# Kernel optimization log

Measured on AMD Instinct MI355X. Metric: run time of the kernel, lower is better.

The kernel has to match this reference:

```python
import jax, jax.numpy as jnp
import numpy as np
from jax import lax

T, H = 4096, 2048          # tokens, hidden_size
E, K = 64, 8               # n_routed_experts, top_k
I = 512                    # moe_intermediate_size
IS = 512                   # shared intermediate = moe_intermediate_size * n_shared_experts
ROUTED_SCALING = 2.5


def setup_inputs() -> dict:
    key = jax.random.key(0)
    ks = jax.random.split(key, 6)
    return {
        "hidden_states": jax.random.normal(ks[0], (T, H), jnp.float32),
        "gate_w": jax.random.normal(ks[1], (H, E), jnp.float32) * 0.05,
        "w13": jax.random.normal(ks[2], (E, H, 2 * I), jnp.float32) * 0.02,
        "w2": jax.random.normal(ks[3], (E, I, H), jnp.float32) * 0.02,
        "shared_w13": jax.random.normal(ks[4], (H, 2 * IS), jnp.float32) * 0.02,
        "shared_w2": jax.random.normal(ks[5], (IS, H), jnp.float32) * 0.02,
    }


def reference(hidden_states, gate_w, w13, w2, shared_w13, shared_w2):
    # --- router: sigmoid scoring, grouped top-k with 1 group == plain top-k ---
    logits = hidden_states @ gate_w                        # [T, E]
    scores = jax.nn.sigmoid(logits.astype(jnp.float32))
    topk_w, topk_ids = lax.top_k(scores, K)                # [T, K]
    topk_w = topk_w / jnp.sum(topk_w, axis=-1, keepdims=True)  # renormalize

    # --- dispatch: sort token-expert pairs by expert id, grouped GEMM ---
    flat_ids = topk_ids.reshape(-1)                        # [T*K]
    order = jnp.argsort(flat_ids)                          # pairs grouped by expert
    token_idx = order // K                                 # source token of each sorted pair
    x_sorted = hidden_states[token_idx]                    # [T*K, H]
    group_sizes = jnp.bincount(flat_ids, length=E).astype(jnp.int32)

    gu = lax.ragged_dot(x_sorted, w13, group_sizes)        # [T*K, 2I]
    h = jax.nn.silu(gu[:, :I]) * gu[:, I:]                 # SiluAndMul
    out_sorted = lax.ragged_dot(h, w2, group_sizes)        # [T*K, H]

    # --- combine: unsort, weight, sum over top-k ---
    inv = jnp.argsort(order)
    out_pairs = out_sorted[inv].reshape(T, K, H)
    routed = jnp.sum(out_pairs * topk_w[..., None].astype(out_pairs.dtype), axis=1)

    # --- shared expert MLP ---
    sg = hidden_states @ shared_w13                        # [T, 2*IS]
    shared = (jax.nn.silu(sg[:, :IS]) * sg[:, IS:]) @ shared_w2

    return routed * ROUTED_SCALING + shared
```

## Files before the change

### kernel.cpp

```cpp
#include <hip/hip_runtime.h>
#include <hip/hip_bf16.h>

#define T_TOK 4096
#define HD    2048
#define NE    64
#define TOPK  8
#define IMID  512
#define N13   1024
#define NPAIR (T_TOK*TOPK)
#define NROWS (NPAIR + T_TOK)
#define MAXT2 208
#define RSCALE 2.5f

typedef __attribute__((ext_vector_type(8))) __bf16 bf16x8;
typedef __attribute__((ext_vector_type(4))) float  f32x4;

__global__ __launch_bounds__(256) void init_kernel(float4* __restrict__ out4,
                                                   int* __restrict__ counts,
                                                   int* __restrict__ curs) {
  int gid = blockIdx.x * 256 + threadIdx.x;
  float4 z; z.x = z.y = z.z = z.w = 0.f;
  out4[gid] = z;
  if (gid < NE + 1) { counts[gid] = 0; curs[gid] = 0; }
}

__global__ __launch_bounds__(256) void cvt_kernel(const float4* __restrict__ hs4,
                                                  bf16x8* __restrict__ hb8) {
  int gid = blockIdx.x * 256 + threadIdx.x;
  float4 a = hs4[2 * gid], b = hs4[2 * gid + 1];
  bf16x8 v = { (__bf16)a.x, (__bf16)a.y, (__bf16)a.z, (__bf16)a.w,
               (__bf16)b.x, (__bf16)b.y, (__bf16)b.z, (__bf16)b.w };
  hb8[gid] = v;
}

__global__ __launch_bounds__(256) void logits_kernel(const float* __restrict__ hs,
                                                     const float* __restrict__ gw,
                                                     float* __restrict__ logits) {
  __shared__ float hsm[64][16];
  __shared__ float gwm[64][64];
  int tid = threadIdx.x;
  int tb = blockIdx.x * 16;
  int tok = tid >> 4, e4 = (tid & 15) * 4;
  float acc[4] = {0.f, 0.f, 0.f, 0.f};
  for (int c = 0; c < 32; ++c) {
    int kb = c * 64;
    {
      int t16 = tid & 15, kq = tid >> 4;
      float4 f = *(const float4*)&hs[(size_t)(tb + t16) * HD + kb + kq * 4];
      hsm[kq * 4 + 0][t16] = f.x; hsm[kq * 4 + 1][t16] = f.y;
      hsm[kq * 4 + 2][t16] = f.z; hsm[kq * 4 + 3][t16] = f.w;
#pragma unroll
      for (int it = 0; it < 4; ++it) {
        int q = tid + it * 256;
        int gr = q >> 4, gc = (q & 15) * 4;
        *(float4*)&gwm[gr][gc] = *(const float4*)&gw[(size_t)(kb + gr) * NE + gc];
      }
    }
    __syncthreads();
#pragma unroll 8
    for (int k = 0; k < 64; ++k) {
      float h = hsm[k][tok];
      float4 g = *(const float4*)&gwm[k][e4];
      acc[0] += h * g.x; acc[1] += h * g.y; acc[2] += h * g.z; acc[3] += h * g.w;
    }
    __syncthreads();
  }
#pragma unroll
  for (int j = 0; j < 4; ++j) logits[(size_t)(tb + tok) * NE + e4 + j] = acc[j];
}

__global__ __launch_bounds__(256) void top8_kernel(const float* __restrict__ logits,
                                                   int* __restrict__ topk_id,
                                                   float* __restrict__ pair_w,
                                                   int* __restrict__ counts) {
  int lane = threadIdx.x & 63;
  int t = blockIdx.x * 4 + (threadIdx.x >> 6);
  float v = logits[(size_t)t * NE + lane];
  float s = 1.f / (1.f + __expf(-v));
  float cur = s, ssum = 0.f;
  int myid = 0; float myw = 0.f;
  for (int k = 0; k < TOPK; ++k) {
    float bv = cur; int bi = lane;
#pragma unroll
    for (int off = 32; off >= 1; off >>= 1) {
      float ov = __shfl_xor(bv, off);
      int   oi = __shfl_xor(bi, off);
      if (ov > bv || (ov == bv && oi < bi)) { bv = ov; bi = oi; }
    }
    ssum += bv;
    if (lane == k) { myid = bi; myw = bv; }
    if (lane == bi) cur = -1.f;
  }
  if (lane < TOPK) {
    topk_id[(size_t)t * TOPK + lane] = myid;
    pair_w[(size_t)t * TOPK + lane] = myw / ssum * RSCALE;
    atomicAdd(&counts[myid], 1);
  }
}

__global__ void scan_kernel(const int* __restrict__ counts, int* __restrict__ offs,
                            int2* __restrict__ tiles) {
  __shared__ int cnt[65], pref[66], tp[66];
  int tid = threadIdx.x;
  if (tid < 64) cnt[tid] = counts[tid];
  if (tid == 64) cnt[64] = T_TOK;
  __syncthreads();
  if (tid == 0) {
    int o = 0, t = 0;
    for (int e = 0; e <= 64; ++e) {
      pref[e] = o; tp[e] = t;
      o += cnt[e]; t += (cnt[e] + 255) >> 8;
    }
    pref[65] = o; tp[65] = t;
  }
  __syncthreads();
  if (tid <= 64) {
    offs[tid] = pref[tid];
    int c = cnt[tid], base = pref[tid], tb = tp[tid];
    int nt = (c + 255) >> 8;
    for (int i = 0; i < nt; ++i) {
      int rr = c - i * 256; if (rr > 256) rr = 256;
      tiles[tb + i] = make_int2(base + i * 256, (tid << 16) | rr);
    }
  }
  __syncthreads();
  for (int i = tp[65] + tid; i < MAXT2; i += 128) tiles[i] = make_int2(0, 0);
}

__global__ __launch_bounds__(256) void scatter_kernel(const int* __restrict__ topk_id,
                                                      const float* __restrict__ pair_w,
                                                      const int* __restrict__ offs,
                                                      int* __restrict__ curs,
                                                      int* __restrict__ row_token,
                                                      float* __restrict__ row_w) {
  int p = blockIdx.x * 256 + threadIdx.x;
  int dst, t; float w;
  if (p < NPAIR) {
    t = p >> 3; int e = topk_id[p]; w = pair_w[p];
    dst = offs[e] + atomicAdd(&curs[e], 1);
  } else {
    t = p - NPAIR; w = 1.0f;
    dst = NPAIR + t;
  }
  row_token[dst] = t;
  row_w[dst] = w;
}

__device__ __forceinline__ int swz(int row, int kbyte) {
  return row * 128 + (kbyte ^ ((row & 7) << 4));
}
__device__ __forceinline__ void glds16(const void* g, void* l) {
  __builtin_amdgcn_global_load_lds((const __attribute__((address_space(1))) void*)g,
                                   (__attribute__((address_space(3))) void*)l, 16, 0, 0);
}
__device__ __forceinline__ void store_bx8(__bf16* Bs, int col, int kbyte, const float* p) {
  bf16x8 v = { (__bf16)p[0], (__bf16)p[1], (__bf16)p[2], (__bf16)p[3],
               (__bf16)p[4], (__bf16)p[5], (__bf16)p[6], (__bf16)p[7] };
  *(bf16x8*)&Bs[swz(col, kbyte) >> 1] = v;
}

__global__ __launch_bounds__(1024, 4) void gemm1_kernel(const __bf16* __restrict__ hidden_bf,
                                                        const float* __restrict__ w13,
                                                        const float* __restrict__ sw13,
                                                        const int* __restrict__ row_token,
                                                        const int2* __restrict__ tiles,
                                                        __bf16* __restrict__ hbuf) {
  int2 td = tiles[blockIdx.y];
  int rows = td.y & 0xFFFF;
  if (rows == 0) return;
  int e = td.y >> 16, row0 = td.x;
  const float* W = (e < NE) ? (w13 + (size_t)e * (HD * N13)) : sw13;
  int n0 = blockIdx.x * 64;

  __shared__ __bf16 As[2][256 * 64];
  __shared__ __bf16 Bgs[2][64 * 64];
  __shared__ __bf16 Bus[2][64 * 64];

  int tid = threadIdx.x;
  int lane = tid & 63, wv = tid >> 6;
  int wrow = wv >> 1, wc = wv & 1;
  int l15 = lane & 15, lq = lane >> 4;

  int kswz = (((lane & 7) ^ ((lane >> 3) & 7)) << 3);
  const __bf16* Abase[2];
#pragma unroll
  for (int i = 0; i < 2; ++i) {
    int grow = row0 + wv * 16 + i * 8 + (lane >> 3);
    if (grow >= NROWS) grow = NROWS - 1;
    Abase[i] = hidden_bf + (size_t)row_token[grow] * HD + kswz;
  }
  int bm = tid >> 9, bcol = tid & 63, bkq = (tid >> 6) & 7;
  const float* Bp0 = W + (size_t)(bkq * 8) * N13 + n0 + bm * 512 + bcol;
  __bf16* Bmy[2];
  Bmy[0] = bm ? Bus[0] : Bgs[0];
  Bmy[1] = bm ? Bus[1] : Bgs[1];

  float p[8];
#pragma unroll
  for (int r = 0; r < 8; ++r) p[r] = Bp0[(size_t)r * N13];
#pragma unroll
  for (int i = 0; i < 2; ++i) glds16(Abase[i], &As[0][wv * 1024 + i * 512]);
  store_bx8(Bmy[0], bcol, bkq * 16, p);
  asm volatile("s_waitcnt vmcnt(0) lgkmcnt(0)" ::: "memory");
  __builtin_amdgcn_s_barrier();
  __builtin_amdgcn_sched_barrier(0);

  f32x4 accg[2][2], accu[2][2];
#pragma unroll
  for (int i = 0; i < 2; ++i)
#pragma unroll
    for (int j = 0; j < 2; ++j) { accg[i][j] = (f32x4)(0.f); accu[i][j] = (f32x4)(0.f); }

  for (int s = 0; s < 32; ++s) {
    int cur = s & 1;
    if (s + 1 < 32) {
      const float* Bp2 = Bp0 + (size_t)(s + 1) * 64 * N13;
#pragma unroll
      for (int r = 0; r < 8; ++r) p[r] = Bp2[(size_t)r * N13];
    }
    __builtin_amdgcn_sched_barrier(0);
    if (s + 1 < 32) {
#pragma unroll
      for (int i = 0; i < 2; ++i)
        glds16(Abase[i] + (s + 1) * 64, &As[cur ^ 1][wv * 1024 + i * 512]);
    }
    __builtin_amdgcn_sched_barrier(0);
#pragma unroll
    for (int kk = 0; kk < 2; ++kk) {
      int koff = kk * 64 + lq * 16;
      bf16x8 a[2], bg[2], bu[2];
#pragma unroll
      for (int i = 0; i < 2; ++i)
        a[i] = *(const bf16x8*)&As[cur][swz(wrow * 32 + i * 16 + l15, koff) >> 1];
#pragma unroll
      for (int j = 0; j < 2; ++j) {
        bg[j] = *(const bf16x8*)&Bgs[cur][swz(wc * 32 + j * 16 + l15, koff) >> 1];
        bu[j] = *(const bf16x8*)&Bus[cur][swz(wc * 32 + j * 16 + l15, koff) >> 1];
      }
#pragma unroll
      for (int i = 0; i < 2; ++i)
#pragma unroll
        for (int j = 0; j < 2; ++j) {
          accg[i][j] = __builtin_amdgcn_mfma_f32_16x16x32_bf16(a[i], bg[j], accg[i][j], 0, 0, 0);
          accu[i][j] = __builtin_amdgcn_mfma_f32_16x16x32_bf16(a[i], bu[j], accu[i][j], 0, 0, 0);
        }
    }
    if (s + 1 < 32)
      store_bx8(Bmy[cur ^ 1], bcol, bkq * 16, p);
    asm volatile("s_waitcnt vmcnt(0) lgkmcnt(0)" ::: "memory");
    __builtin_amdgcn_s_barrier();
    __builtin_amdgcn_sched_barrier(0);
  }
#pragma unroll
  for (int mi = 0; mi < 2; ++mi) {
#pragma unroll
    for (int r = 0; r < 4; ++r) {
      int rl = wrow * 32 + mi * 16 + lq * 4 + r;
      if (rl < rows) {
        size_t hrow = (size_t)(row0 + rl) * IMID;
#pragma unroll
        for (int j = 0; j < 2; ++j) {
          float g = accg[mi][j][r], u = accu[mi][j][r];
          float hv = g * u / (1.f + __expf(-g));
          hbuf[hrow + n0 + wc * 32 + j * 16 + l15] = (__bf16)hv;
        }
      }
    }
  }
}

__global__ __launch_bounds__(1024, 4) void gemm2_kernel(const __bf16* __restrict__ hbuf,
                                                        const float* __restrict__ w2,
                                                        const float* __restrict__ sw2,
                                                        const int* __restrict__ row_token,
                                                        const float* __restrict__ row_w,
                                                        const int2* __restrict__ tiles,
                                                        float* __restrict__ out) {
  int2 td = tiles[blockIdx.y];
  int rows = td.y & 0xFFFF;
  if (rows == 0) return;
  int e = td.y >> 16, row0 = td.x;
  const float* W = (e < NE) ? (w2 + (size_t)e * (IMID * HD)) : sw2;
  int n0 = blockIdx.x * 128;

  __shared__ __bf16 As[2][256 * 64];
  __shared__ __bf16 Bs[2][128 * 64];

  int tid = threadIdx.x;
  int lane = tid & 63, wv = tid >> 6;
  int wr = wv >> 2, wc = wv & 3;
  int l15 = lane & 15, lq = lane >> 4;

  int kswz = (((lane & 7) ^ ((lane >> 3) & 7)) << 3);
  const __bf16* Abase[2];
#pragma unroll
  for (int i = 0; i < 2; ++i) {
    int grow = row0 + wv * 16 + i * 8 + (lane >> 3);
    if (grow >= NROWS) grow = NROWS - 1;
    Abase[i] = hbuf + (size_t)grow * IMID + kswz;
  }
  int bcol = tid & 127, bkq = tid >> 7;
  const float* Bp0 = W + (size_t)(bkq * 8) * HD + n0 + bcol;

  float p[8];
#pragma unroll
  for (int r = 0; r < 8; ++r) p[r] = Bp0[(size_t)r * HD];
#pragma unroll
  for (int i = 0; i < 2; ++i) glds16(Abase[i], &As[0][wv * 1024 + i * 512]);
  store_bx8(Bs[0], bcol, bkq * 16, p);
  asm volatile("s_waitcnt vmcnt(0) lgkmcnt(0)" ::: "memory");
  __builtin_amdgcn_s_barrier();
  __builtin_amdgcn_sched_barrier(0);

  f32x4 acc[4][2];
#pragma unroll
  for (int i = 0; i < 4; ++i)
#pragma unroll
    for (int j = 0; j < 2; ++j) acc[i][j] = (f32x4)(0.f);

  for (int s = 0; s < 8; ++s) {
    int cur = s & 1;
    if (s + 1 < 8) {
      const float* Bp2 = Bp0 + (size_t)(s + 1) * 64 * HD;
#pragma unroll
      for (int r = 0; r < 8; ++r) p[r] = Bp2[(size_t)r * HD];
    }
    __builtin_amdgcn_sched_barrier(0);
    if (s + 1 < 8) {
#pragma unroll
      for (int i = 0; i < 2; ++i)
        glds16(Abase[i] + (s + 1) * 64, &As[cur ^ 1][wv * 1024 + i * 512]);
    }
    __builtin_amdgcn_sched_barrier(0);
#pragma unroll
    for (int kk = 0; kk < 2; ++kk) {
      int koff = kk * 64 + lq * 16;
      bf16x8 a[4], b[2];
#pragma unroll
      for (int i = 0; i < 4; ++i)
        a[i] = *(const bf16x8*)&As[cur][swz(wr * 64 + i * 16 + l15, koff) >> 1];
#pragma unroll
      for (int j = 0; j < 2; ++j)
        b[j] = *(const bf16x8*)&Bs[cur][swz(wc * 32 + j * 16 + l15, koff) >> 1];
#pragma unroll
      for (int i = 0; i < 4; ++i)
#pragma unroll
        for (int j = 0; j < 2; ++j)
          acc[i][j] = __builtin_amdgcn_mfma_f32_16x16x32_bf16(a[i], b[j], acc[i][j], 0, 0, 0);
    }
    if (s + 1 < 8)
      store_bx8(Bs[cur ^ 1], bcol, bkq * 16, p);
    asm volatile("s_waitcnt vmcnt(0) lgkmcnt(0)" ::: "memory");
    __builtin_amdgcn_s_barrier();
    __builtin_amdgcn_sched_barrier(0);
  }
#pragma unroll
  for (int i = 0; i < 4; ++i) {
#pragma unroll
    for (int r = 0; r < 4; ++r) {
      int rl = wr * 64 + i * 16 + lq * 4 + r;
      if (rl < rows) {
        int gr = row0 + rl;
        int tok = row_token[gr];
        float wgt = row_w[gr];
        float* orow = out + (size_t)tok * HD + n0 + wc * 32;
#pragma unroll
        for (int j = 0; j < 2; ++j)
          atomicAdd(&orow[j * 16 + l15], acc[i][j][r] * wgt);
      }
    }
  }
}

extern "C" void kernel_launch(void* const* d_in, const int* in_sizes, int n_in,
                              void* d_out, int out_size, void* d_ws, size_t ws_size,
                              hipStream_t stream) {
  const float* hidden = (const float*)d_in[0];
  const float* gate_w = (const float*)d_in[1];
  const float* w13    = (const float*)d_in[2];
  const float* w2     = (const float*)d_in[3];
  const float* sw13   = (const float*)d_in[4];
  const float* sw2    = (const float*)d_in[5];
  float* out = (float*)d_out;

  char* ws = (char*)d_ws;
  size_t off = 0;
  __bf16* hbuf      = (__bf16*)(ws + off); off += (size_t)NROWS * IMID * 2;
  __bf16* hidden_bf = (__bf16*)(ws + off); off += (size_t)T_TOK * HD * 2;
  float* logits  = (float*)(ws + off);  off += (size_t)T_TOK * NE * 4;
  int*   topk_id = (int*)(ws + off);    off += (size_t)NPAIR * 4;
  float* pair_w  = (float*)(ws + off);  off += (size_t)NPAIR * 4;
  int*   row_tok = (int*)(ws + off);    off += (size_t)NROWS * 4;
  float* row_w   = (float*)(ws + off);  off += (size_t)NROWS * 4;
  int*   counts  = (int*)(ws + off);    off += 512;
  int*   curs    = (int*)(ws + off);    off += 512;
  int*   offs    = (int*)(ws + off);    off += 512;
  int2*  tiles   = (int2*)(ws + off);   off += MAXT2 * 8;

  init_kernel<<<T_TOK * HD / 4 / 256, 256, 0, stream>>>((float4*)out, counts, curs);
  cvt_kernel<<<T_TOK * HD / 8 / 256, 256, 0, stream>>>((const float4*)hidden, (bf16x8*)hidden_bf);
  logits_kernel<<<T_TOK / 16, 256, 0, stream>>>(hidden, gate_w, logits);
  top8_kernel<<<T_TOK / 4, 256, 0, stream>>>(logits, topk_id, pair_w, counts);
  scan_kernel<<<1, 128, 0, stream>>>(counts, offs, tiles);
  scatter_kernel<<<NROWS / 256, 256, 0, stream>>>(topk_id, pair_w, offs, curs, row_tok, row_w);
  gemm1_kernel<<<dim3(8, MAXT2), 1024, 0, stream>>>(hidden_bf, w13, sw13, row_tok, tiles, hbuf);
  gemm2_kernel<<<dim3(16, MAXT2), 1024, 0, stream>>>(hbuf, w2, sw2, row_tok, row_w, tiles, out);
}
```

Before: 848.7 us.

## Widen GEMM N-tiles, switch to 32x32x16 MFMA, and remap blocks per XCD

Both grouped GEMM kernels now use wider N tiles: 128 gate plus 128 up columns in gemm1, and 256 columns in gemm2. They switch from 16x16x32 to 32x32x16 bf16 MFMA with 16-float accumulators. Block indices are remapped so each XCD handles a fixed N slice across tiles, which should improve L2 reuse of expert weights. Wider tiles halve the grid and cut redundant A-row gathers, and setprio raises wave priority around the MFMA section. The cost is more LDS and registers per block, possibly lowering occupancy under launch_bounds(1024,4).

```diff
diff --git a/kernel.cpp b/kernel.cpp
--- a/kernel.cpp
+++ b/kernel.cpp
@@ -12,8 +12,8 @@
 #define MAXT2 208
 #define RSCALE 2.5f
 
-typedef __attribute__((ext_vector_type(8))) __bf16 bf16x8;
-typedef __attribute__((ext_vector_type(4))) float  f32x4;
+typedef __attribute__((ext_vector_type(8)))  __bf16 bf16x8;
+typedef __attribute__((ext_vector_type(16))) float  f32x16;
 
 __global__ __launch_bounds__(256) void init_kernel(float4* __restrict__ out4,
                                                    int* __restrict__ counts,
@@ -165,21 +165,25 @@
                                                         const int* __restrict__ row_token,
                                                         const int2* __restrict__ tiles,
                                                         __bf16* __restrict__ hbuf) {
-  int2 td = tiles[blockIdx.y];
+  int lin = blockIdx.x + 4 * blockIdx.y;
+  int xcd = lin & 7, local = lin >> 3;
+  int ns = xcd & 3;
+  int tix = ((xcd >> 2) * 104) + local;
+  int2 td = tiles[tix];
   int rows = td.y & 0xFFFF;
   if (rows == 0) return;
   int e = td.y >> 16, row0 = td.x;
   const float* W = (e < NE) ? (w13 + (size_t)e * (HD * N13)) : sw13;
-  int n0 = blockIdx.x * 64;
+  int n0 = ns * 128;
 
   __shared__ __bf16 As[2][256 * 64];
-  __shared__ __bf16 Bgs[2][64 * 64];
-  __shared__ __bf16 Bus[2][64 * 64];
+  __shared__ __bf16 Bgs[2][128 * 64];
+  __shared__ __bf16 Bus[2][128 * 64];
 
   int tid = threadIdx.x;
   int lane = tid & 63, wv = tid >> 6;
-  int wrow = wv >> 1, wc = wv & 1;
-  int l15 = lane & 15, lq = lane >> 4;
+  int wr = wv >> 2, wc = wv & 3;
+  int l31 = lane & 31, lh = lane >> 5;
 
   int kswz = (((lane & 7) ^ ((lane >> 3) & 7)) << 3);
   const __bf16* Abase[2];
@@ -189,34 +193,33 @@
     if (grow >= NROWS) grow = NROWS - 1;
     Abase[i] = hidden_bf + (size_t)row_token[grow] * HD + kswz;
   }
-  int bm = tid >> 9, bcol = tid & 63, bkq = (tid >> 6) & 7;
-  const float* Bp0 = W + (size_t)(bkq * 8) * N13 + n0 + bm * 512 + bcol;
-  __bf16* Bmy[2];
-  Bmy[0] = bm ? Bus[0] : Bgs[0];
-  Bmy[1] = bm ? Bus[1] : Bgs[1];
-
-  float p[8];
-#pragma unroll
-  for (int r = 0; r < 8; ++r) p[r] = Bp0[(size_t)r * N13];
+  int bm = tid >> 9, bcol = tid & 127, bkq2 = (tid >> 7) & 3;
+  const float* Bp0 = W + (size_t)(bkq2 * 16) * N13 + (bm ? 512 + n0 : n0) + bcol;
+
+  float p[16];
+#pragma unroll
+  for (int r = 0; r < 16; ++r) p[r] = Bp0[(size_t)r * N13];
 #pragma unroll
   for (int i = 0; i < 2; ++i) glds16(Abase[i], &As[0][wv * 1024 + i * 512]);
-  store_bx8(Bmy[0], bcol, bkq * 16, p);
+  {
+    __bf16* Bmy = bm ? Bus[0] : Bgs[0];
+    store_bx8(Bmy, bcol, bkq2 * 32, p);
+    store_bx8(Bmy, bcol, bkq2 * 32 + 16, p + 8);
+  }
   asm volatile("s_waitcnt vmcnt(0) lgkmcnt(0)" ::: "memory");
   __builtin_amdgcn_s_barrier();
   __builtin_amdgcn_sched_barrier(0);
 
-  f32x4 accg[2][2], accu[2][2];
-#pragma unroll
-  for (int i = 0; i < 2; ++i)
-#pragma unroll
-    for (int j = 0; j < 2; ++j) { accg[i][j] = (f32x4)(0.f); accu[i][j] = (f32x4)(0.f); }
+  f32x16 accg[2], accu[2];
+#pragma unroll
+  for (int i = 0; i < 2; ++i) { accg[i] = (f32x16)(0.f); accu[i] = (f32x16)(0.f); }
 
   for (int s = 0; s < 32; ++s) {
     int cur = s & 1;
     if (s + 1 < 32) {
       const float* Bp2 = Bp0 + (size_t)(s + 1) * 64 * N13;
 #pragma unroll
-      for (int r = 0; r < 8; ++r) p[r] = Bp2[(size_t)r * N13];
+      for (int r = 0; r < 16; ++r) p[r] = Bp2[(size_t)r * N13];
     }
     __builtin_amdgcn_sched_barrier(0);
     if (s + 1 < 32) {
@@ -225,45 +228,39 @@
         glds16(Abase[i] + (s + 1) * 64, &As[cur ^ 1][wv * 1024 + i * 512]);
     }
     __builtin_amdgcn_sched_barrier(0);
-#pragma unroll
-    for (int kk = 0; kk < 2; ++kk) {
-      int koff = kk * 64 + lq * 16;
-      bf16x8 a[2], bg[2], bu[2];
-#pragma unroll
-      for (int i = 0; i < 2; ++i)
-        a[i] = *(const bf16x8*)&As[cur][swz(wrow * 32 + i * 16 + l15, koff) >> 1];
-#pragma unroll
-      for (int j = 0; j < 2; ++j) {
-        bg[j] = *(const bf16x8*)&Bgs[cur][swz(wc * 32 + j * 16 + l15, koff) >> 1];
-        bu[j] = *(const bf16x8*)&Bus[cur][swz(wc * 32 + j * 16 + l15, koff) >> 1];
-      }
-#pragma unroll
-      for (int i = 0; i < 2; ++i)
-#pragma unroll
-        for (int j = 0; j < 2; ++j) {
-          accg[i][j] = __builtin_amdgcn_mfma_f32_16x16x32_bf16(a[i], bg[j], accg[i][j], 0, 0, 0);
-          accu[i][j] = __builtin_amdgcn_mfma_f32_16x16x32_bf16(a[i], bu[j], accu[i][j], 0, 0, 0);
-        }
-    }
-    if (s + 1 < 32)
-      store_bx8(Bmy[cur ^ 1], bcol, bkq * 16, p);
+    __builtin_amdgcn_s_setprio(1);
+#pragma unroll
+    for (int ks = 0; ks < 4; ++ks) {
+      int kbyte = ks * 32 + lh * 16;
+      bf16x8 a0 = *(const bf16x8*)&As[cur][swz(wr * 64 + l31,      kbyte) >> 1];
+      bf16x8 a1 = *(const bf16x8*)&As[cur][swz(wr * 64 + 32 + l31, kbyte) >> 1];
+      bf16x8 bg = *(const bf16x8*)&Bgs[cur][swz(wc * 32 + l31, kbyte) >> 1];
+      bf16x8 bu = *(const bf16x8*)&Bus[cur][swz(wc * 32 + l31, kbyte) >> 1];
+      accg[0] = __builtin_amdgcn_mfma_f32_32x32x16_bf16(a0, bg, accg[0], 0, 0, 0);
+      accg[1] = __builtin_amdgcn_mfma_f32_32x32x16_bf16(a1, bg, accg[1], 0, 0, 0);
+      accu[0] = __builtin_amdgcn_mfma_f32_32x32x16_bf16(a0, bu, accu[0], 0, 0, 0);
+      accu[1] = __builtin_amdgcn_mfma_f32_32x32x16_bf16(a1, bu, accu[1], 0, 0, 0);
+    }
+    __builtin_amdgcn_s_setprio(0);
+    if (s + 1 < 32) {
+      __bf16* Bmy = bm ? Bus[cur ^ 1] : Bgs[cur ^ 1];
+      store_bx8(Bmy, bcol, bkq2 * 32, p);
+      store_bx8(Bmy, bcol, bkq2 * 32 + 16, p + 8);
+    }
     asm volatile("s_waitcnt vmcnt(0) lgkmcnt(0)" ::: "memory");
     __builtin_amdgcn_s_barrier();
     __builtin_amdgcn_sched_barrier(0);
   }
 #pragma unroll
-  for (int mi = 0; mi < 2; ++mi) {
-#pragma unroll
-    for (int r = 0; r < 4; ++r) {
-      int rl = wrow * 32 + mi * 16 + lq * 4 + r;
+  for (int i = 0; i < 2; ++i) {
+#pragma unroll
+    for (int r = 0; r < 16; ++r) {
+      int rloc = (r & 3) + 8 * (r >> 2) + 4 * lh;
+      int rl = wr * 64 + i * 32 + rloc;
       if (rl < rows) {
-        size_t hrow = (size_t)(row0 + rl) * IMID;
-#pragma unroll
-        for (int j = 0; j < 2; ++j) {
-          float g = accg[mi][j][r], u = accu[mi][j][r];
-          float hv = g * u / (1.f + __expf(-g));
-          hbuf[hrow + n0 + wc * 32 + j * 16 + l15] = (__bf16)hv;
-        }
+        float g = accg[i][r], u = accu[i][r];
+        float hv = g * u / (1.f + __expf(-g));
+        hbuf[(size_t)(row0 + rl) * IMID + n0 + wc * 32 + l31] = (__bf16)hv;
       }
     }
   }
@@ -276,20 +273,23 @@
                                                         const float* __restrict__ row_w,
                                                         const int2* __restrict__ tiles,
                                                         float* __restrict__ out) {
-  int2 td = tiles[blockIdx.y];
+  int lin = blockIdx.x + 8 * blockIdx.y;
+  int xcd = lin & 7, local = lin >> 3;
+  int ns = xcd, tix = local;
+  int2 td = tiles[tix];
   int rows = td.y & 0xFFFF;
   if (rows == 0) return;
   int e = td.y >> 16, row0 = td.x;
   const float* W = (e < NE) ? (w2 + (size_t)e * (IMID * HD)) : sw2;
-  int n0 = blockIdx.x * 128;
+  int n0 = ns * 256;
 
   __shared__ __bf16 As[2][256 * 64];
-  __shared__ __bf16 Bs[2][128 * 64];
+  __shared__ __bf16 Bs[2][256 * 64];
 
   int tid = threadIdx.x;
   int lane = tid & 63, wv = tid >> 6;
   int wr = wv >> 2, wc = wv & 3;
-  int l15 = lane & 15, lq = lane >> 4;
+  int l31 = lane & 31, lh = lane >> 5;
 
   int kswz = (((lane & 7) ^ ((lane >> 3) & 7)) << 3);
   const __bf16* Abase[2];
@@ -299,31 +299,32 @@
     if (grow >= NROWS) grow = NROWS - 1;
     Abase[i] = hbuf + (size_t)grow * IMID + kswz;
   }
-  int bcol = tid & 127, bkq = tid >> 7;
-  const float* Bp0 = W + (size_t)(bkq * 8) * HD + n0 + bcol;
-
-  float p[8];
-#pragma unroll
-  for (int r = 0; r < 8; ++r) p[r] = Bp0[(size_t)r * HD];
+  int bcol = tid & 255, bkq2 = tid >> 8;
+  const float* Bp0 = W + (size_t)(bkq2 * 16) * HD + n0 + bcol;
+
+  float p[16];
+#pragma unroll
+  for (int r = 0; r < 16; ++r) p[r] = Bp0[(size_t)r * HD];
 #pragma unroll
   for (int i = 0; i < 2; ++i) glds16(Abase[i], &As[0][wv * 1024 + i * 512]);
-  store_bx8(Bs[0], bcol, bkq * 16, p);
+  store_bx8(Bs[0], bcol, bkq2 * 32, p);
+  store_bx8(Bs[0], bcol, bkq2 * 32 + 16, p + 8);
   asm volatile("s_waitcnt vmcnt(0) lgkmcnt(0)" ::: "memory");
   __builtin_amdgcn_s_barrier();
   __builtin_amdgcn_sched_barrier(0);
 
-  f32x4 acc[4][2];
-#pragma unroll
-  for (int i = 0; i < 4; ++i)
-#pragma unroll
-    for (int j = 0; j < 2; ++j) acc[i][j] = (f32x4)(0.f);
+  f32x16 acc[2][2];
+#pragma unroll
+  for (int i = 0; i < 2; ++i)
+#pragma unroll
+    for (int j = 0; j < 2; ++j) acc[i][j] = (f32x16)(0.f);
 
   for (int s = 0; s < 8; ++s) {
     int cur = s & 1;
     if (s + 1 < 8) {
       const float* Bp2 = Bp0 + (size_t)(s + 1) * 64 * HD;
 #pragma unroll
-      for (int r = 0; r < 8; ++r) p[r] = Bp2[(size_t)r * HD];
+      for (int r = 0; r < 16; ++r) p[r] = Bp2[(size_t)r * HD];
     }
     __builtin_amdgcn_sched_barrier(0);
     if (s + 1 < 8) {
@@ -332,41 +333,41 @@
         glds16(Abase[i] + (s + 1) * 64, &As[cur ^ 1][wv * 1024 + i * 512]);
     }
     __builtin_amdgcn_sched_barrier(0);
-#pragma unroll
-    for (int kk = 0; kk < 2; ++kk) {
-      int koff = kk * 64 + lq * 16;
-      bf16x8 a[4], b[2];
-#pragma unroll
-      for (int i = 0; i < 4; ++i)
-        a[i] = *(const bf16x8*)&As[cur][swz(wr * 64 + i * 16 + l15, koff) >> 1];
-#pragma unroll
-      for (int j = 0; j < 2; ++j)
-        b[j] = *(const bf16x8*)&Bs[cur][swz(wc * 32 + j * 16 + l15, koff) >> 1];
-#pragma unroll
-      for (int i = 0; i < 4; ++i)
-#pragma unroll
-        for (int j = 0; j < 2; ++j)
-          acc[i][j] = __builtin_amdgcn_mfma_f32_16x16x32_bf16(a[i], b[j], acc[i][j], 0, 0, 0);
-    }
-    if (s + 1 < 8)
-      store_bx8(Bs[cur ^ 1], bcol, bkq * 16, p);
+    __builtin_amdgcn_s_setprio(1);
+#pragma unroll
+    for (int ks = 0; ks < 4; ++ks) {
+      int kbyte = ks * 32 + lh * 16;
+      bf16x8 a0 = *(const bf16x8*)&As[cur][swz(wr * 64 + l31,      kbyte) >> 1];
+      bf16x8 a1 = *(const bf16x8*)&As[cur][swz(wr * 64 + 32 + l31, kbyte) >> 1];
+      bf16x8 b0 = *(const bf16x8*)&Bs[cur][swz(wc * 64 + l31,      kbyte) >> 1];
+      bf16x8 b1 = *(const bf16x8*)&Bs[cur][swz(wc * 64 + 32 + l31, kbyte) >> 1];
+      acc[0][0] = __builtin_amdgcn_mfma_f32_32x32x16_bf16(a0, b0, acc[0][0], 0, 0, 0);
+      acc[0][1] = __builtin_amdgcn_mfma_f32_32x32x16_bf16(a0, b1, acc[0][1], 0, 0, 0);
+      acc[1][0] = __builtin_amdgcn_mfma_f32_32x32x16_bf16(a1, b0, acc[1][0], 0, 0, 0);
+      acc[1][1] = __builtin_amdgcn_mfma_f32_32x32x16_bf16(a1, b1, acc[1][1], 0, 0, 0);
+    }
+    __builtin_amdgcn_s_setprio(0);
+    if (s + 1 < 8) {
+      store_bx8(Bs[cur ^ 1], bcol, bkq2 * 32, p);
+      store_bx8(Bs[cur ^ 1], bcol, bkq2 * 32 + 16, p + 8);
+    }
     asm volatile("s_waitcnt vmcnt(0) lgkmcnt(0)" ::: "memory");
     __builtin_amdgcn_s_barrier();
     __builtin_amdgcn_sched_barrier(0);
   }
 #pragma unroll
-  for (int i = 0; i < 4; ++i) {
-#pragma unroll
-    for (int r = 0; r < 4; ++r) {
-      int rl = wr * 64 + i * 16 + lq * 4 + r;
+  for (int i = 0; i < 2; ++i) {
+#pragma unroll
+    for (int r = 0; r < 16; ++r) {
+      int rloc = (r & 3) + 8 * (r >> 2) + 4 * lh;
+      int rl = wr * 64 + i * 32 + rloc;
       if (rl < rows) {
         int gr = row0 + rl;
         int tok = row_token[gr];
         float wgt = row_w[gr];
-        float* orow = out + (size_t)tok * HD + n0 + wc * 32;
-#pragma unroll
-        for (int j = 0; j < 2; ++j)
-          atomicAdd(&orow[j * 16 + l15], acc[i][j][r] * wgt);
+        float* orow = out + (size_t)tok * HD + n0 + wc * 64;
+        atomicAdd(&orow[l31],      acc[i][0][r] * wgt);
+        atomicAdd(&orow[32 + l31], acc[i][1][r] * wgt);
       }
     }
   }
@@ -403,6 +404,6 @@
   top8_kernel<<<T_TOK / 4, 256, 0, stream>>>(logits, topk_id, pair_w, counts);
   scan_kernel<<<1, 128, 0, stream>>>(counts, offs, tiles);
   scatter_kernel<<<NROWS / 256, 256, 0, stream>>>(topk_id, pair_w, offs, curs, row_tok, row_w);
-  gemm1_kernel<<<dim3(8, MAXT2), 1024, 0, stream>>>(hidden_bf, w13, sw13, row_tok, tiles, hbuf);
-  gemm2_kernel<<<dim3(16, MAXT2), 1024, 0, stream>>>(hbuf, w2, sw2, row_tok, row_w, tiles, out);
-}
+  gemm1_kernel<<<dim3(4, MAXT2), 1024, 0, stream>>>(hidden_bf, w13, sw13, row_tok, tiles, hbuf);
+  gemm2_kernel<<<dim3(8, MAXT2), 1024, 0, stream>>>(hbuf, w2, sw2, row_tok, row_w, tiles, out);
+}
```

Result: slower. 894.2 us (+5.4%).

## Triple-buffer A tiles in grouped GEMMs and replace atomic combine with gather kernel

Applied to the files above, without the earlier changes.

Both grouped GEMM kernels now prefetch two k-steps ahead, using three A buffers in LDS and two register sets for B. A partial vmcnt wait replaces the full drain, and MFMA sections run at raised wave priority, so memory latency overlaps compute better. When the workspace is large enough, gemm2 writes weighted per-pair rows to a buffer and a separate combine kernel sums each token's 8 pairs plus the shared row. This removes the float atomics and the output zeroing pass, at the cost of about 300 MB of extra writes and reads and more LDS per block.

```diff
diff --git a/kernel.cpp b/kernel.cpp
--- a/kernel.cpp
+++ b/kernel.cpp
@@ -12,16 +12,15 @@
 #define MAXT2 208
 #define RSCALE 2.5f
 
-typedef __attribute__((ext_vector_type(8))) __bf16 bf16x8;
-typedef __attribute__((ext_vector_type(4))) float  f32x4;
-
-__global__ __launch_bounds__(256) void init_kernel(float4* __restrict__ out4,
-                                                   int* __restrict__ counts,
-                                                   int* __restrict__ curs) {
-  int gid = blockIdx.x * 256 + threadIdx.x;
-  float4 z; z.x = z.y = z.z = z.w = 0.f;
-  out4[gid] = z;
-  if (gid < NE + 1) { counts[gid] = 0; curs[gid] = 0; }
+typedef __attribute__((ext_vector_type(8)))  __bf16 bf16x8;
+typedef __attribute__((ext_vector_type(4)))  float  f32x4;
+
+__global__ void init_small(int* __restrict__ counts, int* __restrict__ curs) {
+  int tid = threadIdx.x;
+  if (tid < NE + 1) { counts[tid] = 0; curs[tid] = 0; }
+}
+__global__ __launch_bounds__(256) void zero_out_kernel(float4* __restrict__ out4) {
+  out4[blockIdx.x * 256 + threadIdx.x] = float4{0.f, 0.f, 0.f, 0.f};
 }
 
 __global__ __launch_bounds__(256) void cvt_kernel(const float4* __restrict__ hs4,
@@ -132,12 +131,14 @@
                                                       const int* __restrict__ offs,
                                                       int* __restrict__ curs,
                                                       int* __restrict__ row_token,
-                                                      float* __restrict__ row_w) {
+                                                      float* __restrict__ row_w,
+                                                      int* __restrict__ inv8) {
   int p = blockIdx.x * 256 + threadIdx.x;
   int dst, t; float w;
   if (p < NPAIR) {
     t = p >> 3; int e = topk_id[p]; w = pair_w[p];
     dst = offs[e] + atomicAdd(&curs[e], 1);
+    inv8[p] = dst;
   } else {
     t = p - NPAIR; w = 1.0f;
     dst = NPAIR + t;
@@ -158,6 +159,43 @@
                (__bf16)p[4], (__bf16)p[5], (__bf16)p[6], (__bf16)p[7] };
   *(bf16x8*)&Bs[swz(col, kbyte) >> 1] = v;
 }
+
+#define G1STEP(S, ACUR, ANX2, BGc, BUc, BGn, BUn, RL, RS)                                  \
+  {                                                                                        \
+    if ((S) + 2 < 32) {                                                                    \
+      const float* Bn_ = Bp0 + (size_t)((S) + 2) * 64 * N13;                               \
+      _Pragma("unroll") for (int r = 0; r < 8; ++r) RL[r] = Bn_[(size_t)r * N13];          \
+      __builtin_amdgcn_sched_barrier(0);                                                   \
+      _Pragma("unroll") for (int i = 0; i < 2; ++i)                                        \
+        glds16(Abase[i] + ((S) + 2) * 64, (ANX2) + wv * 1024 + i * 512);                   \
+    }                                                                                      \
+    __builtin_amdgcn_sched_barrier(0);                                                     \
+    __builtin_amdgcn_s_setprio(1);                                                         \
+    _Pragma("unroll") for (int kk = 0; kk < 2; ++kk) {                                     \
+      int koff = kk * 64 + lq * 16;                                                        \
+      bf16x8 a[2], bg[2], bu[2];                                                           \
+      _Pragma("unroll") for (int i = 0; i < 2; ++i)                                        \
+        a[i] = *(const bf16x8*)&(ACUR)[swz(wrow * 32 + i * 16 + l15, koff) >> 1];          \
+      _Pragma("unroll") for (int j = 0; j < 2; ++j) {                                      \
+        bg[j] = *(const bf16x8*)&(BGc)[swz(wc * 32 + j * 16 + l15, koff) >> 1];            \
+        bu[j] = *(const bf16x8*)&(BUc)[swz(wc * 32 + j * 16 + l15, koff) >> 1];            \
+      }                                                                                    \
+      _Pragma("unroll") for (int i = 0; i < 2; ++i)                                        \
+        _Pragma("unroll") for (int j = 0; j < 2; ++j) {                                    \
+          accg[i][j] = __builtin_amdgcn_mfma_f32_16x16x32_bf16(a[i], bg[j], accg[i][j], 0, 0, 0); \
+          accu[i][j] = __builtin_amdgcn_mfma_f32_16x16x32_bf16(a[i], bu[j], accu[i][j], 0, 0, 0); \
+        }                                                                                  \
+    }                                                                                      \
+    __builtin_amdgcn_s_setprio(0);                                                         \
+    if ((S) + 1 < 32) {                                                                    \
+      __bf16* Bmy_ = bm ? (BUn) : (BGn);                                                   \
+      store_bx8(Bmy_, bcol, bkq * 16, RS);                                                 \
+    }                                                                                      \
+    if ((S) + 2 < 32) asm volatile("s_waitcnt vmcnt(10) lgkmcnt(0)" ::: "memory");         \
+    else              asm volatile("s_waitcnt vmcnt(0) lgkmcnt(0)"  ::: "memory");         \
+    __builtin_amdgcn_s_barrier();                                                          \
+    __builtin_amdgcn_sched_barrier(0);                                                     \
+  }
 
 __global__ __launch_bounds__(1024, 4) void gemm1_kernel(const __bf16* __restrict__ hidden_bf,
                                                         const float* __restrict__ w13,
@@ -172,7 +210,7 @@
   const float* W = (e < NE) ? (w13 + (size_t)e * (HD * N13)) : sw13;
   int n0 = blockIdx.x * 64;
 
-  __shared__ __bf16 As[2][256 * 64];
+  __shared__ __bf16 As0[256 * 64], As1[256 * 64], As2[256 * 64];
   __shared__ __bf16 Bgs[2][64 * 64];
   __shared__ __bf16 Bus[2][64 * 64];
 
@@ -190,18 +228,29 @@
     Abase[i] = hidden_bf + (size_t)row_token[grow] * HD + kswz;
   }
   int bm = tid >> 9, bcol = tid & 63, bkq = (tid >> 6) & 7;
-  const float* Bp0 = W + (size_t)(bkq * 8) * N13 + n0 + bm * 512 + bcol;
-  __bf16* Bmy[2];
-  Bmy[0] = bm ? Bus[0] : Bgs[0];
-  Bmy[1] = bm ? Bus[1] : Bgs[1];
-
-  float p[8];
-#pragma unroll
-  for (int r = 0; r < 8; ++r) p[r] = Bp0[(size_t)r * N13];
-#pragma unroll
-  for (int i = 0; i < 2; ++i) glds16(Abase[i], &As[0][wv * 1024 + i * 512]);
-  store_bx8(Bmy[0], bcol, bkq * 16, p);
-  asm volatile("s_waitcnt vmcnt(0) lgkmcnt(0)" ::: "memory");
+  const float* Bp0 = W + (size_t)(bkq * 8) * N13 + (bm ? 512 + n0 : n0) + bcol;
+
+  float pA[8], pB[8];
+#pragma unroll
+  for (int r = 0; r < 8; ++r) pA[r] = Bp0[(size_t)r * N13];
+  __builtin_amdgcn_sched_barrier(0);
+#pragma unroll
+  for (int i = 0; i < 2; ++i) glds16(Abase[i], As0 + wv * 1024 + i * 512);
+  __builtin_amdgcn_sched_barrier(0);
+  {
+    const float* B1 = Bp0 + (size_t)64 * N13;
+#pragma unroll
+    for (int r = 0; r < 8; ++r) pB[r] = B1[(size_t)r * N13];
+  }
+  __builtin_amdgcn_sched_barrier(0);
+#pragma unroll
+  for (int i = 0; i < 2; ++i) glds16(Abase[i] + 64, As1 + wv * 1024 + i * 512);
+  __builtin_amdgcn_sched_barrier(0);
+  {
+    __bf16* Bmy = bm ? Bus[0] : Bgs[0];
+    store_bx8(Bmy, bcol, bkq * 16, pA);
+  }
+  asm volatile("s_waitcnt vmcnt(10) lgkmcnt(0)" ::: "memory");
   __builtin_amdgcn_s_barrier();
   __builtin_amdgcn_sched_barrier(0);
 
@@ -211,45 +260,12 @@
 #pragma unroll
     for (int j = 0; j < 2; ++j) { accg[i][j] = (f32x4)(0.f); accu[i][j] = (f32x4)(0.f); }
 
-  for (int s = 0; s < 32; ++s) {
-    int cur = s & 1;
-    if (s + 1 < 32) {
-      const float* Bp2 = Bp0 + (size_t)(s + 1) * 64 * N13;
-#pragma unroll
-      for (int r = 0; r < 8; ++r) p[r] = Bp2[(size_t)r * N13];
-    }
-    __builtin_amdgcn_sched_barrier(0);
-    if (s + 1 < 32) {
-#pragma unroll
-      for (int i = 0; i < 2; ++i)
-        glds16(Abase[i] + (s + 1) * 64, &As[cur ^ 1][wv * 1024 + i * 512]);
-    }
-    __builtin_amdgcn_sched_barrier(0);
-#pragma unroll
-    for (int kk = 0; kk < 2; ++kk) {
-      int koff = kk * 64 + lq * 16;
-      bf16x8 a[2], bg[2], bu[2];
-#pragma unroll
-      for (int i = 0; i < 2; ++i)
-        a[i] = *(const bf16x8*)&As[cur][swz(wrow * 32 + i * 16 + l15, koff) >> 1];
-#pragma unroll
-      for (int j = 0; j < 2; ++j) {
-        bg[j] = *(const bf16x8*)&Bgs[cur][swz(wc * 32 + j * 16 + l15, koff) >> 1];
-        bu[j] = *(const bf16x8*)&Bus[cur][swz(wc * 32 + j * 16 + l15, koff) >> 1];
-      }
-#pragma unroll
-      for (int i = 0; i < 2; ++i)
-#pragma unroll
-        for (int j = 0; j < 2; ++j) {
-          accg[i][j] = __builtin_amdgcn_mfma_f32_16x16x32_bf16(a[i], bg[j], accg[i][j], 0, 0, 0);
-          accu[i][j] = __builtin_amdgcn_mfma_f32_16x16x32_bf16(a[i], bu[j], accu[i][j], 0, 0, 0);
-        }
-    }
-    if (s + 1 < 32)
-      store_bx8(Bmy[cur ^ 1], bcol, bkq * 16, p);
-    asm volatile("s_waitcnt vmcnt(0) lgkmcnt(0)" ::: "memory");
-    __builtin_amdgcn_s_barrier();
-    __builtin_amdgcn_sched_barrier(0);
+  __bf16 *Ac = As0, *A1 = As1, *A2 = As2;
+  for (int s = 0; s < 32; s += 2) {
+    G1STEP(s,     Ac, A2, Bgs[0], Bus[0], Bgs[1], Bus[1], pA, pB);
+    { __bf16* t = Ac; Ac = A1; A1 = A2; A2 = t; }
+    G1STEP(s + 1, Ac, A2, Bgs[1], Bus[1], Bgs[0], Bus[0], pB, pA);
+    { __bf16* t = Ac; Ac = A1; A1 = A2; A2 = t; }
   }
 #pragma unroll
   for (int mi = 0; mi < 2; ++mi) {
@@ -269,13 +285,44 @@
   }
 }
 
+#define G2STEP(S, ACUR, ANX2, Bc, Bn, RL, RS)                                              \
+  {                                                                                        \
+    if ((S) + 2 < 8) {                                                                     \
+      const float* Bn_ = Bp0 + (size_t)((S) + 2) * 64 * HD;                                \
+      _Pragma("unroll") for (int r = 0; r < 8; ++r) RL[r] = Bn_[(size_t)r * HD];           \
+      __builtin_amdgcn_sched_barrier(0);                                                   \
+      _Pragma("unroll") for (int i = 0; i < 2; ++i)                                        \
+        glds16(Abase[i] + ((S) + 2) * 64, (ANX2) + wv * 1024 + i * 512);                   \
+    }                                                                                      \
+    __builtin_amdgcn_sched_barrier(0);                                                     \
+    __builtin_amdgcn_s_setprio(1);                                                         \
+    _Pragma("unroll") for (int kk = 0; kk < 2; ++kk) {                                     \
+      int koff = kk * 64 + lq * 16;                                                        \
+      bf16x8 a[4], b[2];                                                                   \
+      _Pragma("unroll") for (int i = 0; i < 4; ++i)                                        \
+        a[i] = *(const bf16x8*)&(ACUR)[swz(wr * 64 + i * 16 + l15, koff) >> 1];            \
+      _Pragma("unroll") for (int j = 0; j < 2; ++j)                                        \
+        b[j] = *(const bf16x8*)&(Bc)[swz(wc * 32 + j * 16 + l15, koff) >> 1];              \
+      _Pragma("unroll") for (int i = 0; i < 4; ++i)                                        \
+        _Pragma("unroll") for (int j = 0; j < 2; ++j)                                      \
+          acc[i][j] = __builtin_amdgcn_mfma_f32_16x16x32_bf16(a[i], b[j], acc[i][j], 0, 0, 0); \
+    }                                                                                      \
+    __builtin_amdgcn_s_setprio(0);                                                         \
+    if ((S) + 1 < 8) store_bx8((Bn), bcol, bkq * 16, RS);                                  \
+    if ((S) + 2 < 8) asm volatile("s_waitcnt vmcnt(10) lgkmcnt(0)" ::: "memory");          \
+    else             asm volatile("s_waitcnt vmcnt(0) lgkmcnt(0)"  ::: "memory");          \
+    __builtin_amdgcn_s_barrier();                                                          \
+    __builtin_amdgcn_sched_barrier(0);                                                     \
+  }
+
+template<int MODE>
 __global__ __launch_bounds__(1024, 4) void gemm2_kernel(const __bf16* __restrict__ hbuf,
                                                         const float* __restrict__ w2,
                                                         const float* __restrict__ sw2,
                                                         const int* __restrict__ row_token,
                                                         const float* __restrict__ row_w,
                                                         const int2* __restrict__ tiles,
-                                                        float* __restrict__ out) {
+                                                        float* __restrict__ dst) {
   int2 td = tiles[blockIdx.y];
   int rows = td.y & 0xFFFF;
   if (rows == 0) return;
@@ -283,7 +330,7 @@
   const float* W = (e < NE) ? (w2 + (size_t)e * (IMID * HD)) : sw2;
   int n0 = blockIdx.x * 128;
 
-  __shared__ __bf16 As[2][256 * 64];
+  __shared__ __bf16 As0[256 * 64], As1[256 * 64], As2[256 * 64];
   __shared__ __bf16 Bs[2][128 * 64];
 
   int tid = threadIdx.x;
@@ -302,13 +349,24 @@
   int bcol = tid & 127, bkq = tid >> 7;
   const float* Bp0 = W + (size_t)(bkq * 8) * HD + n0 + bcol;
 
-  float p[8];
-#pragma unroll
-  for (int r = 0; r < 8; ++r) p[r] = Bp0[(size_t)r * HD];
-#pragma unroll
-  for (int i = 0; i < 2; ++i) glds16(Abase[i], &As[0][wv * 1024 + i * 512]);
-  store_bx8(Bs[0], bcol, bkq * 16, p);
-  asm volatile("s_waitcnt vmcnt(0) lgkmcnt(0)" ::: "memory");
+  float pA[8], pB[8];
+#pragma unroll
+  for (int r = 0; r < 8; ++r) pA[r] = Bp0[(size_t)r * HD];
+  __builtin_amdgcn_sched_barrier(0);
+#pragma unroll
+  for (int i = 0; i < 2; ++i) glds16(Abase[i], As0 + wv * 1024 + i * 512);
+  __builtin_amdgcn_sched_barrier(0);
+  {
+    const float* B1 = Bp0 + (size_t)64 * HD;
+#pragma unroll
+    for (int r = 0; r < 8; ++r) pB[r] = B1[(size_t)r * HD];
+  }
+  __builtin_amdgcn_sched_barrier(0);
+#pragma unroll
+  for (int i = 0; i < 2; ++i) glds16(Abase[i] + 64, As1 + wv * 1024 + i * 512);
+  __builtin_amdgcn_sched_barrier(0);
+  store_bx8(Bs[0], bcol, bkq * 16, pA);
+  asm volatile("s_waitcnt vmcnt(10) lgkmcnt(0)" ::: "memory");
   __builtin_amdgcn_s_barrier();
   __builtin_amdgcn_sched_barrier(0);
 
@@ -318,41 +376,12 @@
 #pragma unroll
     for (int j = 0; j < 2; ++j) acc[i][j] = (f32x4)(0.f);
 
-  for (int s = 0; s < 8; ++s) {
-    int cur = s & 1;
-    if (s + 1 < 8) {
-      const float* Bp2 = Bp0 + (size_t)(s + 1) * 64 * HD;
-#pragma unroll
-      for (int r = 0; r < 8; ++r) p[r] = Bp2[(size_t)r * HD];
-    }
-    __builtin_amdgcn_sched_barrier(0);
-    if (s + 1 < 8) {
-#pragma unroll
-      for (int i = 0; i < 2; ++i)
-        glds16(Abase[i] + (s + 1) * 64, &As[cur ^ 1][wv * 1024 + i * 512]);
-    }
-    __builtin_amdgcn_sched_barrier(0);
-#pragma unroll
-    for (int kk = 0; kk < 2; ++kk) {
-      int koff = kk * 64 + lq * 16;
-      bf16x8 a[4], b[2];
-#pragma unroll
-      for (int i = 0; i < 4; ++i)
-        a[i] = *(const bf16x8*)&As[cur][swz(wr * 64 + i * 16 + l15, koff) >> 1];
-#pragma unroll
-      for (int j = 0; j < 2; ++j)
-        b[j] = *(const bf16x8*)&Bs[cur][swz(wc * 32 + j * 16 + l15, koff) >> 1];
-#pragma unroll
-      for (int i = 0; i < 4; ++i)
-#pragma unroll
-        for (int j = 0; j < 2; ++j)
-          acc[i][j] = __builtin_amdgcn_mfma_f32_16x16x32_bf16(a[i], b[j], acc[i][j], 0, 0, 0);
-    }
-    if (s + 1 < 8)
-      store_bx8(Bs[cur ^ 1], bcol, bkq * 16, p);
-    asm volatile("s_waitcnt vmcnt(0) lgkmcnt(0)" ::: "memory");
-    __builtin_amdgcn_s_barrier();
-    __builtin_amdgcn_sched_barrier(0);
+  __bf16 *Ac = As0, *A1 = As1, *A2 = As2;
+  for (int s = 0; s < 8; s += 2) {
+    G2STEP(s,     Ac, A2, Bs[0], Bs[1], pA, pB);
+    { __bf16* t = Ac; Ac = A1; A1 = A2; A2 = t; }
+    G2STEP(s + 1, Ac, A2, Bs[1], Bs[0], pB, pA);
+    { __bf16* t = Ac; Ac = A1; A1 = A2; A2 = t; }
   }
 #pragma unroll
   for (int i = 0; i < 4; ++i) {
@@ -361,15 +390,46 @@
       int rl = wr * 64 + i * 16 + lq * 4 + r;
       if (rl < rows) {
         int gr = row0 + rl;
-        int tok = row_token[gr];
         float wgt = row_w[gr];
-        float* orow = out + (size_t)tok * HD + n0 + wc * 32;
-#pragma unroll
-        for (int j = 0; j < 2; ++j)
-          atomicAdd(&orow[j * 16 + l15], acc[i][j][r] * wgt);
+        if (MODE == 1) {
+          float* prow = dst + (size_t)gr * HD + n0 + wc * 32;
+#pragma unroll
+          for (int j = 0; j < 2; ++j)
+            prow[j * 16 + l15] = acc[i][j][r] * wgt;
+        } else {
+          int tok = row_token[gr];
+          float* orow = dst + (size_t)tok * HD + n0 + wc * 32;
+#pragma unroll
+          for (int j = 0; j < 2; ++j)
+            atomicAdd(&orow[j * 16 + l15], acc[i][j][r] * wgt);
+        }
       }
     }
   }
+}
+
+__global__ __launch_bounds__(256) void combine_kernel(const float* __restrict__ pairout,
+                                                      const int* __restrict__ inv8,
+                                                      float* __restrict__ out) {
+  int t = blockIdx.x;
+  int c = threadIdx.x * 8;
+  float s0 = 0.f, s1 = 0.f, s2 = 0.f, s3 = 0.f, s4 = 0.f, s5 = 0.f, s6 = 0.f, s7 = 0.f;
+#pragma unroll
+  for (int k = 0; k < 8; ++k) {
+    const float4* pr = (const float4*)(pairout + (size_t)inv8[t * 8 + k] * HD + c);
+    float4 a = pr[0], b = pr[1];
+    s0 += a.x; s1 += a.y; s2 += a.z; s3 += a.w;
+    s4 += b.x; s5 += b.y; s6 += b.z; s7 += b.w;
+  }
+  {
+    const float4* pr = (const float4*)(pairout + (size_t)(NPAIR + t) * HD + c);
+    float4 a = pr[0], b = pr[1];
+    s0 += a.x; s1 += a.y; s2 += a.z; s3 += a.w;
+    s4 += b.x; s5 += b.y; s6 += b.z; s7 += b.w;
+  }
+  float4* o = (float4*)(out + (size_t)t * HD + c);
+  o[0] = float4{s0, s1, s2, s3};
+  o[1] = float4{s4, s5, s6, s7};
 }
 
 extern "C" void kernel_launch(void* const* d_in, const int* in_sizes, int n_in,
@@ -392,17 +452,32 @@
   float* pair_w  = (float*)(ws + off);  off += (size_t)NPAIR * 4;
   int*   row_tok = (int*)(ws + off);    off += (size_t)NROWS * 4;
   float* row_w   = (float*)(ws + off);  off += (size_t)NROWS * 4;
+  int*   inv8    = (int*)(ws + off);    off += (size_t)NPAIR * 4;
   int*   counts  = (int*)(ws + off);    off += 512;
   int*   curs    = (int*)(ws + off);    off += 512;
   int*   offs    = (int*)(ws + off);    off += 512;
   int2*  tiles   = (int2*)(ws + off);   off += MAXT2 * 8;
-
-  init_kernel<<<T_TOK * HD / 4 / 256, 256, 0, stream>>>((float4*)out, counts, curs);
+  off = (off + 255) & ~(size_t)255;
+  float* pairout = (float*)(ws + off);
+  size_t need = off + (size_t)NROWS * HD * 4;
+  bool rows_path = (ws_size >= need);
+
+  init_small<<<1, 256, 0, stream>>>(counts, curs);
+  if (!rows_path)
+    zero_out_kernel<<<T_TOK * HD / 4 / 256, 256, 0, stream>>>((float4*)out);
   cvt_kernel<<<T_TOK * HD / 8 / 256, 256, 0, stream>>>((const float4*)hidden, (bf16x8*)hidden_bf);
   logits_kernel<<<T_TOK / 16, 256, 0, stream>>>(hidden, gate_w, logits);
   top8_kernel<<<T_TOK / 4, 256, 0, stream>>>(logits, topk_id, pair_w, counts);
   scan_kernel<<<1, 128, 0, stream>>>(counts, offs, tiles);
-  scatter_kernel<<<NROWS / 256, 256, 0, stream>>>(topk_id, pair_w, offs, curs, row_tok, row_w);
+  scatter_kernel<<<NROWS / 256, 256, 0, stream>>>(topk_id, pair_w, offs, curs,
+                                                  row_tok, row_w, inv8);
   gemm1_kernel<<<dim3(8, MAXT2), 1024, 0, stream>>>(hidden_bf, w13, sw13, row_tok, tiles, hbuf);
-  gemm2_kernel<<<dim3(16, MAXT2), 1024, 0, stream>>>(hbuf, w2, sw2, row_tok, row_w, tiles, out);
-}
+  if (rows_path) {
+    gemm2_kernel<1><<<dim3(16, MAXT2), 1024, 0, stream>>>(hbuf, w2, sw2, row_tok, row_w,
+                                                          tiles, pairout);
+    combine_kernel<<<T_TOK, 256, 0, stream>>>(pairout, inv8, out);
+  } else {
+    gemm2_kernel<0><<<dim3(16, MAXT2), 1024, 0, stream>>>(hbuf, w2, sw2, row_tok, row_w,
+                                                          tiles, out);
+  }
+}
```

Result: faster. 798.8 us (-5.9%).
